# Performance work log

Measured on AMD Instinct MI355X. Metric: run time of the kernel, lower is better.

The kernel has to match this reference:

```python
import jax, jax.numpy as jnp
import numpy as np


def setup_inputs() -> dict:
    key = jax.random.key(0)
    k1, k2 = jax.random.split(key)
    B, D, H, W = 4, 64, 64, 64
    M = 4096
    z = jax.random.normal(k1, (B, D, H, W), dtype=jnp.float32)
    e = jax.random.normal(k2, (M, D), dtype=jnp.float32)
    log_sigma = jnp.zeros((1,), dtype=jnp.float32)
    return {"z": z, "e": e, "log_sigma": log_sigma}


def reference(z, e, log_sigma):
    # z: [B, D, H, W] latents, e: [M, D] codebook, log_sigma: [1] parameter
    T = 1.0  # latent_temp default
    B, D, H, W = z.shape
    zf = jnp.transpose(z, (0, 2, 3, 1)).reshape(-1, D)  # [N, D]
    N = zf.shape[0]
    # squared pairwise distances via ||z||^2 + ||e||^2 - 2 z e^T (avoids [N,M,D] intermediate)
    d2 = (jnp.sum(zf * zf, axis=1)[:, None]
          + jnp.sum(e * e, axis=1)[None, :]
          - 2.0 * zf @ e.T)  # [N, M]
    alpha = -1.0 / (2.0 * jnp.exp(log_sigma[0]) ** 2)
    matrix = alpha * d2 / T  # [N, M]
    lse = jax.nn.logsumexp(matrix, axis=0)  # [M], reduce over N points per code
    # np.log(np.e) == 1.0
    loss = (-jnp.mean(T * lse)
            + 0.5 * D * (2.0 * log_sigma[0] - 1.0)
            + jnp.log(jnp.asarray(N, dtype=jnp.float32)))
    return loss
```

## Files before the change

kernel.cpp:

```cpp
#include <hip/hip_runtime.h>
#include <hip/hip_bf16.h>
#include <math.h>

#define D_   64
#define HW_  4096
#define N_   16384
#define M_   4096

#define BM 128
#define NSPLIT 32
#define NCHUNK (N_ / NSPLIT)
#define NTILES (NCHUNK / 128)

#define AZN_OFF 0
#define AEN_OFF 16384
#define SUM_OFF 20480
#define ZTB_OFF 24576
#define EBF_OFF (24576 + 524288)
#define WS_FLOATS (EBF_OFF + 131072)

#define L2E 1.4426950408889634f
#define LN2 0.6931471805599453

typedef __attribute__((ext_vector_type(8))) short short8;
typedef __attribute__((ext_vector_type(16))) float floatx16;

#if __has_builtin(__builtin_amdgcn_exp2f)
#define EXP2F(x) __builtin_amdgcn_exp2f(x)
#else
#define EXP2F(x) exp2f(x)
#endif

__device__ __forceinline__ unsigned int bf16_rne(float x) {
    unsigned int u = __float_as_uint(x);
    u += 0x7fffu + ((u >> 16) & 1u);
    return u >> 16;
}

__global__ void prep_kernel(const float* __restrict__ z,
                            const float* __restrict__ e,
                            const float* __restrict__ lsp,
                            float* __restrict__ ws) {
    const float ls = lsp[0];
    const float alpha = -0.5f * __expf(-2.f * ls);
    const float anl = alpha * L2E;
    const float c2p = -2.f * alpha * L2E;
    unsigned char* zTB = (unsigned char*)(ws + ZTB_OFF);
    unsigned char* eB  = (unsigned char*)(ws + EBF_OFF);
    const int blk = blockIdx.x, t = threadIdx.x;

    if (blk < 256) {
        __shared__ float lt[64 * 65];
        const int b = blk >> 6, hw0 = (blk & 63) * 64;
        const int n0 = b * HW_ + hw0;
        const float* zb = z + ((size_t)b * D_) * HW_ + hw0;
#pragma unroll
        for (int i = 0; i < 4; ++i) {
            int idx = t + 256 * i;
            int d = idx >> 4, c = (idx & 15) * 4;
            float4 v = *(const float4*)(zb + (size_t)d * HW_ + c);
            float* p = &lt[d * 65 + c];
            p[0] = v.x; p[1] = v.y; p[2] = v.z; p[3] = v.w;
        }
        __syncthreads();
#pragma unroll
        for (int j = 0; j < 2; ++j) {
            int idx = t + 256 * j;
            int nl = idx >> 3, c = idx & 7;
            float v[8]; float s = 0.f;
#pragma unroll
            for (int jj = 0; jj < 8; ++jj) {
                v[jj] = lt[(8 * c + jj) * 65 + nl];
                s = fmaf(v[jj], v[jj], s);
            }
            s += __shfl_xor(s, 1);
            s += __shfl_xor(s, 2);
            s += __shfl_xor(s, 4);
            uint4 pk;
            pk.x = bf16_rne(v[0] * c2p) | (bf16_rne(v[1] * c2p) << 16);
            pk.y = bf16_rne(v[2] * c2p) | (bf16_rne(v[3] * c2p) << 16);
            pk.z = bf16_rne(v[4] * c2p) | (bf16_rne(v[5] * c2p) << 16);
            pk.w = bf16_rne(v[6] * c2p) | (bf16_rne(v[7] * c2p) << 16);
            const int n = n0 + nl;
            *(uint4*)(zTB + (size_t)(n >> 5) * 4096
                          + (c >> 1) * 1024 + (c & 1) * 512 + (n & 31) * 16) = pk;
            if (c == 0) ws[AZN_OFF + n] = anl * s;
        }
    } else {
        int m = (blk - 256) * 256 + t;
        const float4* ep = (const float4*)(e + (size_t)m * D_);
        float s = 0.f;
        unsigned int pk[32];
#pragma unroll
        for (int k = 0; k < 16; ++k) {
            float4 v = ep[k];
            s += v.x * v.x + v.y * v.y + v.z * v.z + v.w * v.w;
            pk[2 * k]     = bf16_rne(v.x) | (bf16_rne(v.y) << 16);
            pk[2 * k + 1] = bf16_rne(v.z) | (bf16_rne(v.w) << 16);
        }
        unsigned char* gb = eB + (size_t)(m >> 5) * 4096 + (m & 31) * 16;
#pragma unroll
        for (int c = 0; c < 8; ++c)
            *(uint4*)(gb + (c >> 1) * 1024 + (c & 1) * 512) =
                make_uint4(pk[4 * c], pk[4 * c + 1], pk[4 * c + 2], pk[4 * c + 3]);
        ws[AEN_OFF + m] = anl * s;
        ws[SUM_OFF + m] = 0.f;
    }
}

__global__ __launch_bounds__(256, 2) void main_fast(float* __restrict__ ws) {
    __shared__ float lds_red[BM];
    const unsigned char* zTB = (const unsigned char*)(ws + ZTB_OFF);
    const unsigned char* eB  = (const unsigned char*)(ws + EBF_OFF);
    const float* azn = ws + AZN_OFF;
    float* sums = ws + SUM_OFF;

    const int m0 = blockIdx.x * BM;
    const int ns = blockIdx.y;
    const int t = threadIdx.x;
    const int lane = t & 63;
    const int w = t >> 6;
    const int rlo = lane & 31;
    const int kh = lane >> 5;

    const unsigned char* ebase = eB + ((size_t)m0 >> 5) * 4096 + lane * 16;
    short8 bf[4][4];
#pragma unroll
    for (int mt = 0; mt < 4; ++mt)
#pragma unroll
        for (int ks = 0; ks < 4; ++ks)
            bf[mt][ks] = *(const short8*)(ebase + mt * 4096 + ks * 1024);

    float sum[4] = {0.f, 0.f, 0.f, 0.f};
    const int nbase = ns * NCHUNK + w * 32;
    const unsigned char* abase = zTB + ((size_t)nbase >> 5) * 4096 + lane * 16;

    short8 afc[4];
    float4 aznc[4];
    {
#pragma unroll
        for (int ks = 0; ks < 4; ++ks)
            afc[ks] = *(const short8*)(abase + ks * 1024);
        const int r0 = nbase + 4 * kh;
#pragma unroll
        for (int rg = 0; rg < 4; ++rg) aznc[rg] = *(const float4*)(azn + r0 + 8 * rg);
    }

#pragma unroll
    for (int tile = 0; tile < NTILES; ++tile) {
        short8 afn[4];
        float4 aznn[4];
        if (tile + 1 < NTILES) {
            const unsigned char* ab = abase + (size_t)(tile + 1) * 16384;
#pragma unroll
            for (int ks = 0; ks < 4; ++ks)
                afn[ks] = *(const short8*)(ab + ks * 1024);
            const int r0 = nbase + (tile + 1) * 128 + 4 * kh;
#pragma unroll
            for (int rg = 0; rg < 4; ++rg) aznn[rg] = *(const float4*)(azn + r0 + 8 * rg);
        }

        float azn_r[16];
#pragma unroll
        for (int rg = 0; rg < 4; ++rg) {
            azn_r[rg * 4 + 0] = aznc[rg].x; azn_r[rg * 4 + 1] = aznc[rg].y;
            azn_r[rg * 4 + 2] = aznc[rg].z; azn_r[rg * 4 + 3] = aznc[rg].w;
        }

        floatx16 acc[4];
#pragma unroll
        for (int mt = 0; mt < 4; ++mt)
#pragma unroll
            for (int r = 0; r < 16; ++r)
                acc[mt][r] = azn_r[r];

#pragma unroll
        for (int ks = 0; ks < 4; ++ks)
#pragma unroll
            for (int mt = 0; mt < 4; ++mt)
                acc[mt] = __builtin_amdgcn_mfma_f32_32x32x16_bf16(
                    afc[ks], bf[mt][ks], acc[mt], 0, 0, 0);

#pragma unroll
        for (int mt = 0; mt < 4; ++mt) {
            float s = 0.f;
#pragma unroll
            for (int r = 0; r < 16; ++r) s += EXP2F(acc[mt][r]);
            sum[mt] += s;
        }

#pragma unroll
        for (int ks = 0; ks < 4; ++ks) afc[ks] = afn[ks];
#pragma unroll
        for (int rg = 0; rg < 4; ++rg) aznc[rg] = aznn[rg];
    }

#pragma unroll
    for (int mt = 0; mt < 4; ++mt) sum[mt] += __shfl_down(sum[mt], 32);

    if (t < BM) lds_red[t] = 0.f;
    __syncthreads();
    if (lane < 32) {
#pragma unroll
        for (int mt = 0; mt < 4; ++mt) atomicAdd(&lds_red[mt * 32 + rlo], sum[mt]);
    }
    __syncthreads();
    if (t < BM) atomicAdd(&sums[m0 + t], lds_red[t]);
}

__global__ void finalize_fast(const float* __restrict__ ws,
                              const float* __restrict__ lsp,
                              float* __restrict__ out) {
    __shared__ double red[256];
    const float* sums = ws + SUM_OFF;
    const float* aen = ws + AEN_OFF;
    int t = threadIdx.x;
    double local = 0.0;
#pragma unroll
    for (int j = 0; j < 16; ++j) {
        int m = t + 256 * j;
        local += (double)(aen[m] + log2f(sums[m]));
    }
    red[t] = local;
    __syncthreads();
    for (int off = 128; off > 0; off >>= 1) {
        if (t < off) red[t] += red[t + off];
        __syncthreads();
    }
    if (t == 0) {
        double ls = (double)lsp[0];
        double loss = -(LN2 * red[0] / (double)M_)
                      + 0.5 * (double)D_ * (2.0 * ls - 1.0)
                      + log((double)N_);
        out[0] = (float)loss;
    }
}

extern "C" void kernel_launch(void* const* d_in, const int* in_sizes, int n_in,
                              void* d_out, int out_size, void* d_ws, size_t ws_size,
                              hipStream_t stream) {
    const float* z   = (const float*)d_in[0];
    const float* e   = (const float*)d_in[1];
    const float* lsp = (const float*)d_in[2];
    float* ws  = (float*)d_ws;
    float* out = (float*)d_out;

    hipLaunchKernelGGL(prep_kernel, dim3(272), dim3(256), 0, stream, z, e, lsp, ws);
    hipLaunchKernelGGL(main_fast, dim3(M_ / BM, NSPLIT), dim3(256), 0, stream, ws);
    hipLaunchKernelGGL(finalize_fast, dim3(1), dim3(256), 0, stream, ws, lsp, out);
}
```

Before: 77.32 us.

## Fuse finalize into main kernel via last-block ticket, split prep finer, drop prefetch

```diff
diff --git a/kernel.cpp b/kernel.cpp
--- a/kernel.cpp
+++ b/kernel.cpp
@@ -11,13 +11,15 @@
 #define NSPLIT 32
 #define NCHUNK (N_ / NSPLIT)
 #define NTILES (NCHUNK / 128)
+#define NBLOCKS ((M_ / BM) * NSPLIT)
 
 #define AZN_OFF 0
 #define AEN_OFF 16384
 #define SUM_OFF 20480
 #define ZTB_OFF 24576
 #define EBF_OFF (24576 + 524288)
-#define WS_FLOATS (EBF_OFF + 131072)
+#define TICK_OFF (EBF_OFF + 131072)
+#define WS_FLOATS (TICK_OFF + 1)
 
 #define L2E 1.4426950408889634f
 #define LN2 0.6931471805599453
@@ -49,28 +51,26 @@
     unsigned char* eB  = (unsigned char*)(ws + EBF_OFF);
     const int blk = blockIdx.x, t = threadIdx.x;
 
-    if (blk < 256) {
-        __shared__ float lt[64 * 65];
-        const int b = blk >> 6, hw0 = (blk & 63) * 64;
+    if (blk < 512) {
+        __shared__ float lt[64 * 33];
+        const int b = blk >> 7, hw0 = (blk & 127) * 32;
         const int n0 = b * HW_ + hw0;
         const float* zb = z + ((size_t)b * D_) * HW_ + hw0;
 #pragma unroll
-        for (int i = 0; i < 4; ++i) {
+        for (int i = 0; i < 2; ++i) {
             int idx = t + 256 * i;
-            int d = idx >> 4, c = (idx & 15) * 4;
+            int d = idx >> 3, c = (idx & 7) * 4;
             float4 v = *(const float4*)(zb + (size_t)d * HW_ + c);
-            float* p = &lt[d * 65 + c];
+            float* p = &lt[d * 33 + c];
             p[0] = v.x; p[1] = v.y; p[2] = v.z; p[3] = v.w;
         }
         __syncthreads();
-#pragma unroll
-        for (int j = 0; j < 2; ++j) {
-            int idx = t + 256 * j;
-            int nl = idx >> 3, c = idx & 7;
+        {
+            int nl = t >> 3, c = t & 7;
             float v[8]; float s = 0.f;
 #pragma unroll
             for (int jj = 0; jj < 8; ++jj) {
-                v[jj] = lt[(8 * c + jj) * 65 + nl];
+                v[jj] = lt[(8 * c + jj) * 33 + nl];
                 s = fmaf(v[jj], v[jj], s);
             }
             s += __shfl_xor(s, 1);
@@ -87,7 +87,7 @@
             if (c == 0) ws[AZN_OFF + n] = anl * s;
         }
     } else {
-        int m = (blk - 256) * 256 + t;
+        int m = (blk - 512) * 256 + t;
         const float4* ep = (const float4*)(e + (size_t)m * D_);
         float s = 0.f;
         unsigned int pk[32];
@@ -105,11 +105,17 @@
                 make_uint4(pk[4 * c], pk[4 * c + 1], pk[4 * c + 2], pk[4 * c + 3]);
         ws[AEN_OFF + m] = anl * s;
         ws[SUM_OFF + m] = 0.f;
-    }
-}
-
-__global__ __launch_bounds__(256, 2) void main_fast(float* __restrict__ ws) {
-    __shared__ float lds_red[BM];
+        if (blk == 512 && t == 0) *(int*)(ws + TICK_OFF) = 0;
+    }
+}
+
+__global__ __launch_bounds__(256, 2) void main_fast(float* __restrict__ ws,
+                                                    const float* __restrict__ lsp,
+                                                    float* __restrict__ out) {
+    __shared__ double red[256];
+    __shared__ int lastFlag;
+    float* lds_red = (float*)red;
+
     const unsigned char* zTB = (const unsigned char*)(ws + ZTB_OFF);
     const unsigned char* eB  = (const unsigned char*)(ws + EBF_OFF);
     const float* azn = ws + AZN_OFF;
@@ -135,36 +141,21 @@
     const int nbase = ns * NCHUNK + w * 32;
     const unsigned char* abase = zTB + ((size_t)nbase >> 5) * 4096 + lane * 16;
 
-    short8 afc[4];
-    float4 aznc[4];
-    {
+#pragma unroll
+    for (int tile = 0; tile < NTILES; ++tile) {
+        const unsigned char* ab = abase + (size_t)tile * 16384;
+        short8 af[4];
 #pragma unroll
         for (int ks = 0; ks < 4; ++ks)
-            afc[ks] = *(const short8*)(abase + ks * 1024);
-        const int r0 = nbase + 4 * kh;
-#pragma unroll
-        for (int rg = 0; rg < 4; ++rg) aznc[rg] = *(const float4*)(azn + r0 + 8 * rg);
-    }
-
-#pragma unroll
-    for (int tile = 0; tile < NTILES; ++tile) {
-        short8 afn[4];
-        float4 aznn[4];
-        if (tile + 1 < NTILES) {
-            const unsigned char* ab = abase + (size_t)(tile + 1) * 16384;
-#pragma unroll
-            for (int ks = 0; ks < 4; ++ks)
-                afn[ks] = *(const short8*)(ab + ks * 1024);
-            const int r0 = nbase + (tile + 1) * 128 + 4 * kh;
-#pragma unroll
-            for (int rg = 0; rg < 4; ++rg) aznn[rg] = *(const float4*)(azn + r0 + 8 * rg);
-        }
-
+            af[ks] = *(const short8*)(ab + ks * 1024);
+
+        const int r0 = nbase + tile * 128 + 4 * kh;
         float azn_r[16];
 #pragma unroll
         for (int rg = 0; rg < 4; ++rg) {
-            azn_r[rg * 4 + 0] = aznc[rg].x; azn_r[rg * 4 + 1] = aznc[rg].y;
-            azn_r[rg * 4 + 2] = aznc[rg].z; azn_r[rg * 4 + 3] = aznc[rg].w;
+            float4 a4 = *(const float4*)(azn + r0 + 8 * rg);
+            azn_r[rg * 4 + 0] = a4.x; azn_r[rg * 4 + 1] = a4.y;
+            azn_r[rg * 4 + 2] = a4.z; azn_r[rg * 4 + 3] = a4.w;
         }
 
         floatx16 acc[4];
@@ -179,7 +170,7 @@
 #pragma unroll
             for (int mt = 0; mt < 4; ++mt)
                 acc[mt] = __builtin_amdgcn_mfma_f32_32x32x16_bf16(
-                    afc[ks], bf[mt][ks], acc[mt], 0, 0, 0);
+                    af[ks], bf[mt][ks], acc[mt], 0, 0, 0);
 
 #pragma unroll
         for (int mt = 0; mt < 4; ++mt) {
@@ -188,11 +179,6 @@
             for (int r = 0; r < 16; ++r) s += EXP2F(acc[mt][r]);
             sum[mt] += s;
         }
-
-#pragma unroll
-        for (int ks = 0; ks < 4; ++ks) afc[ks] = afn[ks];
-#pragma unroll
-        for (int rg = 0; rg < 4; ++rg) aznc[rg] = aznn[rg];
     }
 
 #pragma unroll
@@ -206,33 +192,36 @@
     }
     __syncthreads();
     if (t < BM) atomicAdd(&sums[m0 + t], lds_red[t]);
-}
-
-__global__ void finalize_fast(const float* __restrict__ ws,
-                              const float* __restrict__ lsp,
-                              float* __restrict__ out) {
-    __shared__ double red[256];
-    const float* sums = ws + SUM_OFF;
-    const float* aen = ws + AEN_OFF;
-    int t = threadIdx.x;
-    double local = 0.0;
-#pragma unroll
-    for (int j = 0; j < 16; ++j) {
-        int m = t + 256 * j;
-        local += (double)(aen[m] + log2f(sums[m]));
-    }
-    red[t] = local;
-    __syncthreads();
-    for (int off = 128; off > 0; off >>= 1) {
-        if (t < off) red[t] += red[t + off];
+
+    __syncthreads();
+    if (t == 0) {
+        int old = atomicAdd((int*)(ws + TICK_OFF), 1);
+        lastFlag = (old == NBLOCKS - 1);
+    }
+    __syncthreads();
+
+    if (lastFlag) {
+        const float* aen = ws + AEN_OFF;
+        double local = 0.0;
+#pragma unroll
+        for (int j = 0; j < 16; ++j) {
+            int m = t + 256 * j;
+            float S = atomicAdd(&sums[m], 0.f);
+            local += (double)(aen[m] + log2f(S));
+        }
+        red[t] = local;
         __syncthreads();
-    }
-    if (t == 0) {
-        double ls = (double)lsp[0];
-        double loss = -(LN2 * red[0] / (double)M_)
-                      + 0.5 * (double)D_ * (2.0 * ls - 1.0)
-                      + log((double)N_);
-        out[0] = (float)loss;
+        for (int off = 128; off > 0; off >>= 1) {
+            if (t < off) red[t] += red[t + off];
+            __syncthreads();
+        }
+        if (t == 0) {
+            double ls = (double)lsp[0];
+            double loss = -(LN2 * red[0] / (double)M_)
+                          + 0.5 * (double)D_ * (2.0 * ls - 1.0)
+                          + log((double)N_);
+            out[0] = (float)loss;
+        }
     }
 }
 
@@ -245,7 +234,7 @@
     float* ws  = (float*)d_ws;
     float* out = (float*)d_out;
 
-    hipLaunchKernelGGL(prep_kernel, dim3(272), dim3(256), 0, stream, z, e, lsp, ws);
-    hipLaunchKernelGGL(main_fast, dim3(M_ / BM, NSPLIT), dim3(256), 0, stream, ws);
-    hipLaunchKernelGGL(finalize_fast, dim3(1), dim3(256), 0, stream, ws, lsp, out);
-}
+    hipLaunchKernelGGL(prep_kernel, dim3(528), dim3(256), 0, stream, z, e, lsp, ws);
+    hipLaunchKernelGGL(main_fast, dim3(M_ / BM, NSPLIT), dim3(256), 0, stream,
+                       ws, lsp, out);
+}
```

New measurement: 83.12 us. 1.08x slower.
